# Performance work log

Measured on AMD Instinct MI355X. Metric: run time of the kernel, lower is better.

The kernel has to match this reference:

```python
import jax, jax.numpy as jnp
import numpy as np

B, S, L, D = 64, 4, 64, 64
R = L  # n_rules defaults to L
F1 = S * L * D  # 16384 flattened features into the FFN


def setup_inputs() -> dict:
    key = jax.random.key(0)
    ks = jax.random.split(key, 10)
    return {
        "x": jax.random.normal(ks[0], (B, S, L, D), jnp.float32),
        # to_q: Linear(D, D)
        "Wq": jax.random.normal(ks[1], (D, D), jnp.float32) / np.sqrt(D),
        "bq": jnp.zeros((D,), jnp.float32),
        # fuzzy rule centers / widths (torch.rand -> uniform[0,1))
        "centers": jax.random.uniform(ks[2], (R, D), jnp.float32),
        "widths": jax.random.uniform(ks[3], (R, D), jnp.float32) + 0.1,
        # to_c: Linear(D, R*D)
        "Wc": jax.random.normal(ks[4], (R * D, D), jnp.float32) / np.sqrt(D),
        "bc": jnp.zeros((R * D,), jnp.float32),
        # LayerNorm over [S, R, D]
        "ln_g": jnp.ones((S, L, D), jnp.float32),
        "ln_b": jnp.zeros((S, L, D), jnp.float32),
        # FFN
        "W1": jax.random.normal(ks[5], (F1 // 2, F1), jnp.float32) / np.sqrt(F1),
        "b1": jnp.zeros((F1 // 2,), jnp.float32),
        "W2": jax.random.normal(ks[6], (64, F1 // 2), jnp.float32) / np.sqrt(F1 // 2),
        "b2": jnp.zeros((64,), jnp.float32),
        "W3": jax.random.normal(ks[7], (2, 64), jnp.float32) / np.sqrt(64),
        "b3": jnp.zeros((2,), jnp.float32),
    }


def reference(x, Wq, bq, centers, widths, Wc, bc, ln_g, ln_b, W1, b1, W2, b2, W3, b3):
    b, s, c, t = x.shape  # [B, S, L, D]
    # projection to_q applied per (b s c) row of length D
    q = x @ Wq.T + bq  # [B,S,L,D]
    # fuzzy membership: z[...,r] = mean_d(-0.5 * (|q - center_r| / width_r)^2)
    diff = jnp.abs(q[..., None, :] - centers)          # [B,S,L,R,D]
    z = jnp.mean(-0.5 * jnp.square(diff / widths), axis=-1)  # [B,S,L,R]
    Fss = jax.nn.softmax(z, axis=-1)                   # firing strengths over rules
    # consequents: Linear(D, R*D) then view as [..., D, R] (einops '(t r)')
    conq = (x @ Wc.T + bc).reshape(b, s, c, t, R)      # [B,S,L,D,R]
    # rule-weighted combination: out[...,t] = sum_r conq[...,t,r] * Fss[...,r]
    attn = jnp.einsum('bsldr,bslr->bsld', conq, Fss)   # [B,S,L,D]
    # LayerNorm over [S, R, D] jointly (normalized_shape=[S, n_rules, D])
    h = x + attn
    mu = h.mean(axis=(1, 2, 3), keepdims=True)
    var = h.var(axis=(1, 2, 3), keepdims=True)
    hn = (h - mu) * jax.lax.rsqrt(var + 1e-5) * ln_g + ln_b
    # FFN head
    f = hn.reshape(b, -1)                              # [B, S*L*D]
    f = jax.nn.relu(f @ W1.T + b1)
    f = jax.nn.relu(f @ W2.T + b2)
    return f @ W3.T + b3                               # [B, 2]
```

## Files before the change

kernel.cpp:

```cpp
#include <hip/hip_runtime.h>
#include <hip/hip_bf16.h>


__device__ __forceinline__ float b2f(unsigned short v){
  union { unsigned u; float f; } c; c.u = ((unsigned)v) << 16; return c.f;
}

__device__ __forceinline__ unsigned short f2b(float f){
  __hip_bfloat16 b = __float2bfloat16(f);
  return *reinterpret_cast<unsigned short*>(&b);
}

template<bool BF>
__device__ __forceinline__ float ldg1(const void* p, int i){
  if constexpr (BF) return b2f(((const unsigned short*)p)[i]);
  else return ((const float*)p)[i];
}

template<bool BF>
__device__ __forceinline__ float4 ldg4(const void* p, int i){
  if constexpr (BF){
    ushort4 u = *(const ushort4*)(((const unsigned short*)p) + i);
    return make_float4(b2f(u.x), b2f(u.y), b2f(u.z), b2f(u.w));
  } else {
    return *(const float4*)(((const float*)p) + i);
  }
}

__device__ __forceinline__ bool detect_bf16(const void* lng){
  return ((const unsigned*)lng)[0] != 0x3F800000u;
}

typedef __attribute__((ext_vector_type(8))) short bf16x8;
typedef __attribute__((ext_vector_type(4))) float f32x4;

__device__ __forceinline__ void gll16(const void* g, void* l){
  __builtin_amdgcn_global_load_lds(
      (const __attribute__((address_space(1))) unsigned*)g,
      (__attribute__((address_space(3))) unsigned*)l, 16, 0, 0);
}

template<bool BF>
__device__ void fss_body(const void* x, const void* Wq, const void* bq,
                         const void* cen, const void* wid, float* fss){
  __shared__ float xs[64];
  __shared__ float qs[64];
  int t = threadIdx.x;
  int row = blockIdx.x;
  xs[t] = ldg1<BF>(x, row*64 + t);
  __syncthreads();
  float acc = ldg1<BF>(bq, t);
  #pragma unroll
  for (int d4 = 0; d4 < 16; d4++){
    float4 wv = ldg4<BF>(Wq, t*64 + d4*4);
    float4 xv = *(float4*)&xs[d4*4];
    acc += wv.x*xv.x + wv.y*xv.y + wv.z*xv.z + wv.w*xv.w;
  }
  qs[t] = acc;
  __syncthreads();
  float zs = 0.f;
  #pragma unroll
  for (int d4 = 0; d4 < 16; d4++){
    float4 cv = ldg4<BF>(cen, t*64 + d4*4);
    float4 wv = ldg4<BF>(wid, t*64 + d4*4);
    float4 qv = *(float4*)&qs[d4*4];
    float e0 = __fdividef(qv.x - cv.x, wv.x);
    float e1 = __fdividef(qv.y - cv.y, wv.y);
    float e2 = __fdividef(qv.z - cv.z, wv.z);
    float e3 = __fdividef(qv.w - cv.w, wv.w);
    zs += e0*e0 + e1*e1 + e2*e2 + e3*e3;
  }
  float z = zs * (-0.5f / 64.f);
  float m = z;
  #pragma unroll
  for (int off = 32; off; off >>= 1) m = fmaxf(m, __shfl_xor(m, off));
  float e = expf(z - m);
  float s = e;
  #pragma unroll
  for (int off = 32; off; off >>= 1) s += __shfl_xor(s, off);
  fss[row*64 + t] = __fdividef(e, s);
}

__global__ void __launch_bounds__(64)
k_fss(const void* x, const void* Wq, const void* bq, const void* cen,
      const void* wid, const void* lng, float* fss){
  if (detect_bf16(lng)) fss_body<true>(x, Wq, bq, cen, wid, fss);
  else                  fss_body<false>(x, Wq, bq, cen, wid, fss);
}

template<bool BF>
__device__ void attn_body(const void* x, const void* Wc, const void* bc,
                          const float* fss, float* h, float* stats){
  __shared__ float lx[64][68];
  __shared__ float lw[64][68];
  __shared__ float lf[64][65];
  __shared__ float sred[8];
  int tid  = threadIdx.x;
  int row0 = blockIdx.x * 64;
  {
    int rl = tid >> 2, seg = tid & 3;
    #pragma unroll
    for (int j4 = 0; j4 < 4; j4++){
      int d = seg*4 + j4*16;
      float4 v = ldg4<BF>(x, (row0+rl)*64 + d);
      *(float4*)&lx[rl][d] = v;
      float4 f = *(const float4*)&fss[(row0+rl)*64 + d];
      lf[rl][d+0] = f.x; lf[rl][d+1] = f.y; lf[rl][d+2] = f.z; lf[rl][d+3] = f.w;
    }
  }
  __syncthreads();
  int tx = tid & 15, ty = tid >> 4;
  int t0 = tx*4, m0 = ty*4;
  float C[4][4];
  #pragma unroll
  for (int i = 0; i < 4; i++)
    #pragma unroll
    for (int j = 0; j < 4; j++) C[i][j] = 0.f;

  int st = tid >> 2, sseg = tid & 3;
  for (int r = 0; r < 64; r++){
    #pragma unroll
    for (int j4 = 0; j4 < 4; j4++){
      int d = sseg*4 + j4*16;
      *(float4*)&lw[st][d] = ldg4<BF>(Wc, st*4096 + r*64 + d);
    }
    __syncthreads();
    float w[4];
    #pragma unroll
    for (int i = 0; i < 4; i++) w[i] = lf[m0+i][r];
    float S[4][4];
    #pragma unroll
    for (int i = 0; i < 4; i++)
      #pragma unroll
      for (int j = 0; j < 4; j++) S[i][j] = 0.f;
    #pragma unroll
    for (int d4 = 0; d4 < 16; d4++){
      float4 a[4], bb[4];
      #pragma unroll
      for (int i = 0; i < 4; i++) a[i]  = *(float4*)&lx[m0+i][d4*4];
      #pragma unroll
      for (int j = 0; j < 4; j++) bb[j] = *(float4*)&lw[t0+j][d4*4];
      #pragma unroll
      for (int i = 0; i < 4; i++)
        #pragma unroll
        for (int j = 0; j < 4; j++)
          S[i][j] += a[i].x*bb[j].x + a[i].y*bb[j].y + a[i].z*bb[j].z + a[i].w*bb[j].w;
    }
    #pragma unroll
    for (int j = 0; j < 4; j++){
      float bcv = ldg1<BF>(bc, (t0+j)*64 + r);
      #pragma unroll
      for (int i = 0; i < 4; i++)
        C[i][j] += w[i] * (S[i][j] + bcv);
    }
    __syncthreads();
  }
  float lsum = 0.f, lsq = 0.f;
  #pragma unroll
  for (int i = 0; i < 4; i++){
    float4 hv;
    hv.x = lx[m0+i][t0+0] + C[i][0];
    hv.y = lx[m0+i][t0+1] + C[i][1];
    hv.z = lx[m0+i][t0+2] + C[i][2];
    hv.w = lx[m0+i][t0+3] + C[i][3];
    *(float4*)&h[(row0+m0+i)*64 + t0] = hv;
    lsum += hv.x + hv.y + hv.z + hv.w;
    lsq  += hv.x*hv.x + hv.y*hv.y + hv.z*hv.z + hv.w*hv.w;
  }
  #pragma unroll
  for (int off = 32; off; off >>= 1){
    lsum += __shfl_xor(lsum, off);
    lsq  += __shfl_xor(lsq,  off);
  }
  int lane = tid & 63, wid = tid >> 6;
  if (lane == 0){ sred[wid] = lsum; sred[4+wid] = lsq; }
  __syncthreads();
  if (tid == 0){
    float s  = sred[0] + sred[1] + sred[2] + sred[3];
    float s2 = sred[4] + sred[5] + sred[6] + sred[7];
    int b = blockIdx.x >> 2;
    atomicAdd(&stats[b*2 + 0], s);
    atomicAdd(&stats[b*2 + 1], s2);
  }
}

__global__ void __launch_bounds__(256)
k_attn(const void* x, const void* Wc, const void* bc, const void* lng,
       const float* fss, float* h, float* stats){
  if (detect_bf16(lng)) attn_body<true>(x, Wc, bc, fss, h, stats);
  else                  attn_body<false>(x, Wc, bc, fss, h, stats);
}

template<bool BF>
__device__ void norm_body(const float* h, const float* stats, const void* g,
                          const void* be, void* hn){
  int gid = blockIdx.x * 256 + threadIdx.x;
  int e0  = gid * 4;
  int b   = e0 >> 14;
  int i   = e0 & 16383;
  float s  = stats[b*2 + 0];
  float s2 = stats[b*2 + 1];
  float mu  = s * (1.f/16384.f);
  float var = s2 * (1.f/16384.f) - mu*mu;
  float rs  = rsqrtf(var + 1e-5f);
  float4 hv = *(const float4*)&h[e0];
  float4 gv = ldg4<BF>(g, i);
  float4 bv = ldg4<BF>(be, i);
  float o0 = (hv.x - mu)*rs*gv.x + bv.x;
  float o1 = (hv.y - mu)*rs*gv.y + bv.y;
  float o2 = (hv.z - mu)*rs*gv.z + bv.z;
  float o3 = (hv.w - mu)*rs*gv.w + bv.w;
  if constexpr (BF){
    ushort4 u;
    u.x = f2b(o0); u.y = f2b(o1); u.z = f2b(o2); u.w = f2b(o3);
    *(ushort4*)&((unsigned short*)hn)[e0] = u;
  } else {
    float4 o; o.x = o0; o.y = o1; o.z = o2; o.w = o3;
    *(float4*)&((float*)hn)[e0] = o;
  }
}

__global__ void __launch_bounds__(256)
k_norm(const float* h, const float* stats, const void* g, const void* be,
       const void* lng, void* hn){
  if (detect_bf16(lng)) norm_body<true>(h, stats, g, be, hn);
  else                  norm_body<false>(h, stats, g, be, hn);
}


__device__ __forceinline__ void stage64(const unsigned short* gbase,
                                        unsigned short* lbase, int tid){
  #pragma unroll
  for (int i = 0; i < 2; i++){
    int row = i*32 + (tid >> 3);
    int ss  = (tid & 7) ^ (row & 7);
    gll16(gbase + row*16384 + ss*8, lbase + i*2048 + tid*8);
  }
}

__device__ void ffn1_mfma(const unsigned short* hnb, const unsigned short* w1,
                          float* f1, char* smem){
  unsigned short* s = (unsigned short*)smem;
  const int tid = threadIdx.x;
  const int bx  = blockIdx.x;
  const int n0  = (bx >> 2) * 64;
  const int kc0 = (bx & 3) * 4096;
  const unsigned short* gA = hnb + kc0;
  const unsigned short* gB = w1 + (size_t)n0*16384 + kc0;

  stage64(gA, s, tid);
  stage64(gB, s + 4096, tid);
  __syncthreads();

  const int lane = tid & 63;
  const int l15 = lane & 15, l4 = lane >> 4;
  const int w  = tid >> 6;
  const int wm = w & 1, wn = w >> 1;
  const int mrow0 = wm*32 + l15, mrow1 = wm*32 + 16 + l15;
  const int nrow0 = wn*32 + l15, nrow1 = wn*32 + 16 + l15;

  f32x4 acc[2][2];
  #pragma unroll
  for (int i = 0; i < 2; i++)
    #pragma unroll
    for (int j = 0; j < 2; j++)
      #pragma unroll
      for (int r = 0; r < 4; r++)
        acc[i][j][r] = 0.f;

  for (int t = 0; t < 64; t++){
    unsigned short* A  = s + (t & 1)*8192;
    unsigned short* Bt = A + 4096;
    if (t < 63){
      unsigned short* nxt = s + ((t+1) & 1)*8192;
      stage64(gA + (t+1)*64, nxt, tid);
      stage64(gB + (t+1)*64, nxt + 4096, tid);
    }
    #pragma unroll
    for (int kk = 0; kk < 2; kk++){
      int slot = kk*4 + l4;
      bf16x8 af0 = *(const bf16x8*)(A  + mrow0*64 + ((slot ^ (mrow0 & 7)) << 3));
      bf16x8 af1 = *(const bf16x8*)(A  + mrow1*64 + ((slot ^ (mrow1 & 7)) << 3));
      bf16x8 bf0 = *(const bf16x8*)(Bt + nrow0*64 + ((slot ^ (nrow0 & 7)) << 3));
      bf16x8 bf1 = *(const bf16x8*)(Bt + nrow1*64 + ((slot ^ (nrow1 & 7)) << 3));
      acc[0][0] = __builtin_amdgcn_mfma_f32_16x16x32_bf16(af0, bf0, acc[0][0], 0, 0, 0);
      acc[0][1] = __builtin_amdgcn_mfma_f32_16x16x32_bf16(af0, bf1, acc[0][1], 0, 0, 0);
      acc[1][0] = __builtin_amdgcn_mfma_f32_16x16x32_bf16(af1, bf0, acc[1][0], 0, 0, 0);
      acc[1][1] = __builtin_amdgcn_mfma_f32_16x16x32_bf16(af1, bf1, acc[1][1], 0, 0, 0);
    }
    __syncthreads();
  }

  #pragma unroll
  for (int i = 0; i < 2; i++){
    int rbase = wm*32 + i*16 + l4*4;
    #pragma unroll
    for (int j = 0; j < 2; j++){
      int col = n0 + wn*32 + j*16 + l15;
      #pragma unroll
      for (int r = 0; r < 4; r++)
        atomicAdd(&f1[(rbase + r)*8192 + col], acc[i][j][r]);
    }
  }
}

__device__ void ffn1_body_f32(const float* hn, const void* W1, float* f1,
                              char* smem){
  float (*la)[68] = (float(*)[68])smem;
  float (*lb)[68] = (float(*)[68])(smem + 17408);
  int tid = threadIdx.x;
  int nt = blockIdx.x >> 1, kh = blockIdx.x & 1;
  int n0 = nt * 32;
  int tx = tid & 15, ty = tid >> 4;
  int nl0 = tx*2, m0 = ty*4;
  float C[4][2];
  #pragma unroll
  for (int i = 0; i < 4; i++){ C[i][0] = 0.f; C[i][1] = 0.f; }
  int rl = tid >> 2, seg = tid & 3;
  int wl = tid >> 3, s8  = tid & 7;
  int kbeg = kh * 8192;
  for (int kc = kbeg; kc < kbeg + 8192; kc += 64){
    #pragma unroll
    for (int j4 = 0; j4 < 4; j4++){
      int d = seg*4 + j4*16;
      *(float4*)&la[rl][d] = *(const float4*)&hn[rl*16384 + kc + d];
    }
    #pragma unroll
    for (int j4 = 0; j4 < 2; j4++){
      int d = s8*4 + j4*32;
      *(float4*)&lb[wl][d] = ldg4<false>(W1, (n0+wl)*16384 + kc + d);
    }
    __syncthreads();
    #pragma unroll
    for (int d4 = 0; d4 < 16; d4++){
      float4 a[4], bb[2];
      #pragma unroll
      for (int i = 0; i < 4; i++) a[i]  = *(float4*)&la[m0+i][d4*4];
      #pragma unroll
      for (int j = 0; j < 2; j++) bb[j] = *(float4*)&lb[nl0+j][d4*4];
      #pragma unroll
      for (int i = 0; i < 4; i++)
        #pragma unroll
        for (int j = 0; j < 2; j++)
          C[i][j] += a[i].x*bb[j].x + a[i].y*bb[j].y + a[i].z*bb[j].z + a[i].w*bb[j].w;
    }
    __syncthreads();
  }
  #pragma unroll
  for (int i = 0; i < 4; i++)
    #pragma unroll
    for (int j = 0; j < 2; j++)
      atomicAdd(&f1[(m0+i)*8192 + n0 + nl0 + j], C[i][j]);
}

__global__ void __launch_bounds__(256)
k_ffn1(const void* hn, const void* W1, const void* lng, float* f1){
  __shared__ __align__(16) char smem[32768];
  if (detect_bf16(lng))
    ffn1_mfma((const unsigned short*)hn, (const unsigned short*)W1, f1, smem);
  else
    ffn1_body_f32((const float*)hn, W1, f1, smem);
}

template<bool BF>
__device__ void ffn23_body(const float* f1, const void* b1, const void* W2,
                           const void* b2, const void* W3, const void* b3,
                           void* out){
  __shared__ float sf[8192];
  __shared__ float p[4][64];
  __shared__ float sf2[64];
  int m = blockIdx.x, tid = threadIdx.x;
  #pragma unroll
  for (int j4 = 0; j4 < 8; j4++){
    int k = tid*4 + j4*1024;
    float4 v  = *(const float4*)&f1[m*8192 + k];
    float4 bb = ldg4<BF>(b1, k);
    sf[k+0] = fmaxf(v.x + bb.x, 0.f);
    sf[k+1] = fmaxf(v.y + bb.y, 0.f);
    sf[k+2] = fmaxf(v.z + bb.z, 0.f);
    sf[k+3] = fmaxf(v.w + bb.w, 0.f);
  }
  __syncthreads();
  int n = tid & 63, kq = tid >> 6;
  float acc = 0.f;
  for (int k = kq*2048; k < kq*2048 + 2048; k += 4){
    float4 wv = ldg4<BF>(W2, n*8192 + k);
    float4 sv = *(const float4*)&sf[k];
    acc += wv.x*sv.x + wv.y*sv.y + wv.z*sv.z + wv.w*sv.w;
  }
  p[kq][n] = acc;
  __syncthreads();
  if (tid < 64){
    float t = p[0][tid] + p[1][tid] + p[2][tid] + p[3][tid] + ldg1<BF>(b2, tid);
    sf2[tid] = fmaxf(t, 0.f);
  }
  __syncthreads();
  if (tid < 2){
    float acc2 = ldg1<BF>(b3, tid);
    for (int nn = 0; nn < 64; nn++)
      acc2 += sf2[nn] * ldg1<BF>(W3, tid*64 + nn);
    if constexpr (BF) ((__hip_bfloat16*)out)[m*2 + tid] = __float2bfloat16(acc2);
    else              ((float*)out)[m*2 + tid] = acc2;
  }
}

__global__ void __launch_bounds__(256)
k_ffn23(const float* f1, const void* b1, const void* W2, const void* b2,
        const void* W3, const void* b3, const void* lng, void* out){
  if (detect_bf16(lng)) ffn23_body<true>(f1, b1, W2, b2, W3, b3, out);
  else                  ffn23_body<false>(f1, b1, W2, b2, W3, b3, out);
}

extern "C" void kernel_launch(void* const* d_in, const int* in_sizes, int n_in,
                              void* d_out, int out_size, void* d_ws, size_t ws_size,
                              hipStream_t stream){
  const void* x       = d_in[0];
  const void* Wq      = d_in[1];
  const void* bq      = d_in[2];
  const void* centers = d_in[3];
  const void* widths  = d_in[4];
  const void* Wc      = d_in[5];
  const void* bc      = d_in[6];
  const void* ln_g    = d_in[7];
  const void* ln_b    = d_in[8];
  const void* W1      = d_in[9];
  const void* b1      = d_in[10];
  const void* W2      = d_in[11];
  const void* b2      = d_in[12];
  const void* W3      = d_in[13];
  const void* b3      = d_in[14];

  float* ws    = (float*)d_ws;
  float* fss   = ws + 0;
  float* h     = ws + 1048576;
  float* hn    = ws + 2097152;
  float* f1    = ws + 3145728;
  float* stats = ws + 3670016;

  hipMemsetAsync(f1, 0, (524288 + 128) * sizeof(float), stream);
  k_fss  <<<16384,  64, 0, stream>>>(x, Wq, bq, centers, widths, ln_g, fss);
  k_attn <<<  256, 256, 0, stream>>>(x, Wc, bc, ln_g, fss, h, stats);
  k_norm <<< 1024, 256, 0, stream>>>(h, stats, ln_g, ln_b, ln_g, hn);
  k_ffn1 <<<  512, 256, 0, stream>>>(hn, W1, ln_g, f1);
  k_ffn23<<<   64, 256, 0, stream>>>(f1, b1, W2, b2, W3, b3, ln_g, d_out);
}
```

Before: 1.431 ms.

## Retile fp32 FFN1 GEMM to 64x256 blocks with 8x8 register tiles and swizzled LDS

Replaces the fp32 fallback FFN1 kernel, which used 64x32 output tiles with 4x2 per-thread tiles and a K split of 2, with 64x256 tiles, 8x8 per-thread register tiles and a K split of 16 over 32-wide K steps. The W1 tile in LDS gets an XOR swizzle to avoid bank conflicts. This raises arithmetic intensity per LDS load and per global load of hn. In exchange it uses more registers and LDS and issues more atomicAdd partial sums into f1. The launch grid must match the new block-index decomposition, which is not visible here.

```diff
diff --git a/kernel.cpp b/kernel.cpp
--- a/kernel.cpp
+++ b/kernel.cpp
@@ -227,7 +227,6 @@
   else                  norm_body<false>(h, stats, g, be, hn);
 }
 
-
 __device__ __forceinline__ void stage64(const unsigned short* gbase,
                                         unsigned short* lbase, int tid){
   #pragma unroll
@@ -304,62 +303,73 @@
   }
 }
 
-__device__ void ffn1_body_f32(const float* hn, const void* W1, float* f1,
-                              char* smem){
-  float (*la)[68] = (float(*)[68])smem;
-  float (*lb)[68] = (float(*)[68])(smem + 17408);
-  int tid = threadIdx.x;
-  int nt = blockIdx.x >> 1, kh = blockIdx.x & 1;
-  int n0 = nt * 32;
-  int tx = tid & 15, ty = tid >> 4;
-  int nl0 = tx*2, m0 = ty*4;
-  float C[4][2];
-  #pragma unroll
-  for (int i = 0; i < 4; i++){ C[i][0] = 0.f; C[i][1] = 0.f; }
-  int rl = tid >> 2, seg = tid & 3;
-  int wl = tid >> 3, s8  = tid & 7;
-  int kbeg = kh * 8192;
-  for (int kc = kbeg; kc < kbeg + 8192; kc += 64){
-    #pragma unroll
-    for (int j4 = 0; j4 < 4; j4++){
-      int d = seg*4 + j4*16;
-      *(float4*)&la[rl][d] = *(const float4*)&hn[rl*16384 + kc + d];
-    }
-    #pragma unroll
-    for (int j4 = 0; j4 < 2; j4++){
-      int d = s8*4 + j4*32;
-      *(float4*)&lb[wl][d] = ldg4<false>(W1, (n0+wl)*16384 + kc + d);
+__device__ void ffn1_f32(const float* hn, const float* W1, float* f1,
+                         char* smem){
+  float* As = (float*)smem;
+  float* Bs = (float*)(smem + 8192);
+  const int tid = threadIdx.x;
+  const int bx  = blockIdx.x;
+  const int n0  = (bx >> 4) * 256;
+  const int k0  = (bx & 15) * 1024;
+  const int txx = tid & 31, ty = tid >> 5;
+  const int m0  = ty * 8;
+  const int sw  = txx & 7;
+  const int srow = tid >> 3, sc = tid & 7;
+
+  float C[8][8];
+  #pragma unroll
+  for (int i = 0; i < 8; i++)
+    #pragma unroll
+    for (int j = 0; j < 8; j++) C[i][j] = 0.f;
+
+  for (int s = 0; s < 32; s++){
+    int kg = k0 + s*32;
+    #pragma unroll
+    for (int r = 0; r < 2; r++){
+      int m = r*32 + srow;
+      *(float4*)&As[m*32 + sc*4] =
+          *(const float4*)&hn[m*16384 + kg + sc*4];
+    }
+    #pragma unroll
+    for (int r = 0; r < 8; r++){
+      int n = r*32 + srow;
+      int slot = sc ^ ((n >> 3) & 7);
+      *(float4*)&Bs[n*32 + slot*4] =
+          *(const float4*)&W1[(size_t)(n0+n)*16384 + kg + sc*4];
     }
     __syncthreads();
     #pragma unroll
-    for (int d4 = 0; d4 < 16; d4++){
-      float4 a[4], bb[2];
-      #pragma unroll
-      for (int i = 0; i < 4; i++) a[i]  = *(float4*)&la[m0+i][d4*4];
-      #pragma unroll
-      for (int j = 0; j < 2; j++) bb[j] = *(float4*)&lb[nl0+j][d4*4];
-      #pragma unroll
-      for (int i = 0; i < 4; i++)
+    for (int g = 0; g < 8; g++){
+      float4 a[8], bv[8];
+      #pragma unroll
+      for (int i = 0; i < 8; i++)
+        a[i] = *(const float4*)&As[(m0+i)*32 + g*4];
+      #pragma unroll
+      for (int j = 0; j < 8; j++)
+        bv[j] = *(const float4*)&Bs[(txx*8+j)*32 + ((g ^ sw) << 2)];
+      #pragma unroll
+      for (int i = 0; i < 8; i++)
         #pragma unroll
-        for (int j = 0; j < 2; j++)
-          C[i][j] += a[i].x*bb[j].x + a[i].y*bb[j].y + a[i].z*bb[j].z + a[i].w*bb[j].w;
+        for (int j = 0; j < 8; j++)
+          C[i][j] += a[i].x*bv[j].x + a[i].y*bv[j].y
+                   + a[i].z*bv[j].z + a[i].w*bv[j].w;
     }
     __syncthreads();
   }
   #pragma unroll
-  for (int i = 0; i < 4; i++)
-    #pragma unroll
-    for (int j = 0; j < 2; j++)
-      atomicAdd(&f1[(m0+i)*8192 + n0 + nl0 + j], C[i][j]);
+  for (int i = 0; i < 8; i++)
+    #pragma unroll
+    for (int j = 0; j < 8; j++)
+      atomicAdd(&f1[(m0+i)*8192 + n0 + txx*8 + j], C[i][j]);
 }
 
 __global__ void __launch_bounds__(256)
 k_ffn1(const void* hn, const void* W1, const void* lng, float* f1){
-  __shared__ __align__(16) char smem[32768];
+  __shared__ __align__(16) char smem[40960];
   if (detect_bf16(lng))
     ffn1_mfma((const unsigned short*)hn, (const unsigned short*)W1, f1, smem);
   else
-    ffn1_body_f32((const float*)hn, W1, f1, smem);
+    ffn1_f32((const float*)hn, (const float*)W1, f1, smem);
 }
 
 template<bool BF>
```

Result: slower. 3.032 ms (+111.9%).
